# Kernel tuning notes

Hardware: AMD Instinct MI355X
Metric: run time of the kernel (lower is better)

Reference implementation:

```python
import jax, jax.numpy as jnp
import numpy as np

N, E = 50000, 1600000
IN_DIM, EMBED, OUT = 512, 128, 64


def setup_inputs() -> dict:
    key = jax.random.key(0)
    k = jax.random.split(key, 8)
    x = jax.random.normal(k[0], (N, IN_DIM), dtype=jnp.float32)
    edge_index = jax.random.randint(k[1], (2, E), 0, N, dtype=jnp.int32)
    W_dense = jax.random.normal(k[2], (EMBED, IN_DIM), dtype=jnp.float32) * 0.02
    b_dense = jnp.zeros((EMBED,), dtype=jnp.float32)
    W_gat = jax.random.normal(k[3], (OUT, EMBED), dtype=jnp.float32) * 0.05
    att_src = jax.random.normal(k[4], (OUT,), dtype=jnp.float32) * 0.1
    att_dst = jax.random.normal(k[5], (OUT,), dtype=jnp.float32) * 0.1
    b_gat = jnp.zeros((OUT,), dtype=jnp.float32)
    return {"x": x, "edge_index": edge_index, "W_dense": W_dense, "b_dense": b_dense,
            "W_gat": W_gat, "att_src": att_src, "att_dst": att_dst, "b_gat": b_gat}


def reference(x, edge_index, W_dense, b_dense, W_gat, att_src, att_dst, b_gat):
    # dense -> LeakyReLU(0.01) (nn.LeakyReLU default)
    h = jax.nn.leaky_relu(x @ W_dense.T + b_dense, negative_slope=0.01)  # [N, EMBED]
    n = h.shape[0]
    # GATConv (PyG, heads=1, add_self_loops=True, negative_slope=0.2)
    loops = jnp.arange(n, dtype=edge_index.dtype)
    src = jnp.concatenate([edge_index[0], loops])
    dst = jnp.concatenate([edge_index[1], loops])
    g = h @ W_gat.T  # [N, OUT]
    a_src = g @ att_src  # [N]
    a_dst = g @ att_dst  # [N]
    e = jax.nn.leaky_relu(a_src[src] + a_dst[dst], negative_slope=0.2)  # [E+N]
    # segment softmax over destination neighborhoods (self loops guarantee non-empty)
    m = jax.ops.segment_max(e, dst, num_segments=n)
    e = jnp.exp(e - m[dst])
    denom = jax.ops.segment_sum(e, dst, num_segments=n)
    alpha = e / denom[dst]
    out = jax.ops.segment_sum(g[src] * alpha[:, None], dst, num_segments=n) + b_gat
    # original returns ([embed_x], [embed_x]); we return the single embedding tensor
    return out
```

## Files before the change

### kernel.cpp

```cpp
#include <hip/hip_runtime.h>
#include <math.h>

#define IN_DIM 512
#define EMBED 128
#define OUT_DIM 64
#define NBPAD 256
#define SEGSH 12
#define CAP_LDS 10240

typedef __attribute__((ext_vector_type(8))) short bf16x8;
typedef __attribute__((ext_vector_type(4))) float f32x4;

__device__ __forceinline__ float lrelu(float v, float s) { return v > 0.f ? v : v * s; }

__device__ __forceinline__ float readlane_f(float v, int l) {
  return __int_as_float(__builtin_amdgcn_readlane(__float_as_int(v), l));
}

__device__ __forceinline__ unsigned short f2bf(float f) {
  unsigned int u = __float_as_uint(f);
  u += 0x7fff + ((u >> 16) & 1);
  return (unsigned short)(u >> 16);
}
__device__ __forceinline__ float bf2f(unsigned short h) {
  return __uint_as_float(((unsigned int)h) << 16);
}

__device__ __forceinline__ unsigned int cvt_pk_bf16(float a, float b) {
  unsigned int r;
  asm("v_cvt_pk_bf16_f32 %0, %1, %2" : "=v"(r) : "v"(a), "v"(b));
  return r;
}

#define LDA 40

__global__ __launch_bounds__(256) void split_w_kernel(
    const float* __restrict__ W, unsigned short* __restrict__ Wh,
    unsigned short* __restrict__ Wl, int total) {
  int i = (blockIdx.x * 256 + threadIdx.x) * 4;
  if (i >= total) return;
  float4 v = *(const float4*)(W + i);
  unsigned int h0 = cvt_pk_bf16(v.x, v.y);
  unsigned int h1 = cvt_pk_bf16(v.z, v.w);
  float r0 = v.x - __uint_as_float(h0 << 16);
  float r1 = v.y - __uint_as_float(h0 & 0xffff0000u);
  float r2 = v.z - __uint_as_float(h1 << 16);
  float r3 = v.w - __uint_as_float(h1 & 0xffff0000u);
  unsigned int l0 = cvt_pk_bf16(r0, r1);
  unsigned int l1 = cvt_pk_bf16(r2, r3);
  uint2 hh = make_uint2(h0, h1);
  uint2 ll = make_uint2(l0, l1);
  *(uint2*)(Wh + i) = hh;
  *(uint2*)(Wl + i) = ll;
}

__global__ __launch_bounds__(256) void gemm1_mfma_kernel(
    const float* __restrict__ x, const unsigned short* __restrict__ Wdh,
    const unsigned short* __restrict__ Wdl, const float* __restrict__ bd,
    float* __restrict__ h, int N) {
  __shared__ __align__(16) unsigned short Ah[64][LDA];
  __shared__ __align__(16) unsigned short Al[64][LDA];
  __shared__ __align__(16) unsigned short Bh[64][LDA];
  __shared__ __align__(16) unsigned short Bl[64][LDA];

  const int tid = threadIdx.x;
  const int lane = tid & 63;
  const int wid = tid >> 6;
  const int wr = wid >> 1, wc = wid & 1;
  const int mblk = blockIdx.x * 64;
  const int nblk = blockIdx.y * 64;
  const int quad = lane >> 4;
  const int l15 = lane & 15;

  const int arow = tid >> 2, acb = (tid & 3) * 8;
  const bool avalid = (mblk + arow) < N;
  const float* aptr = x + (size_t)(mblk + arow) * IN_DIM + acb;
  const unsigned short* bhp = Wdh + (size_t)(nblk + arow) * IN_DIM + acb;
  const unsigned short* blp = Wdl + (size_t)(nblk + arow) * IN_DIM + acb;

  f32x4 acc[2][2];
#pragma unroll
  for (int i = 0; i < 2; ++i)
#pragma unroll
    for (int j = 0; j < 2; ++j) acc[i][j] = (f32x4){0.f, 0.f, 0.f, 0.f};

  float4 t0, t1;
  uint4 bhv, blv;
  auto do_load = [&](int k0) {
    if (avalid) {
      t0 = *(const float4*)(aptr + k0);
      t1 = *(const float4*)(aptr + k0 + 4);
    } else {
      t0 = t1 = make_float4(0.f, 0.f, 0.f, 0.f);
    }
    bhv = *(const uint4*)(bhp + k0);
    blv = *(const uint4*)(blp + k0);
  };
  do_load(0);

  for (int k0 = 0; k0 < IN_DIM; k0 += 32) {
    float av[8] = {t0.x, t0.y, t0.z, t0.w, t1.x, t1.y, t1.z, t1.w};
    union { unsigned int u[4]; uint4 v; } AHI, ALO;
#pragma unroll
    for (int i = 0; i < 4; ++i) {
      unsigned int hp = cvt_pk_bf16(av[2 * i], av[2 * i + 1]);
      float r0 = av[2 * i] - __uint_as_float(hp << 16);
      float r1 = av[2 * i + 1] - __uint_as_float(hp & 0xffff0000u);
      AHI.u[i] = hp;
      ALO.u[i] = cvt_pk_bf16(r0, r1);
    }

    __syncthreads();
    *(uint4*)&Ah[arow][acb] = AHI.v;
    *(uint4*)&Al[arow][acb] = ALO.v;
    *(uint4*)&Bh[arow][acb] = bhv;
    *(uint4*)&Bl[arow][acb] = blv;
    __syncthreads();

    if (k0 + 32 < IN_DIM) do_load(k0 + 32);

    bf16x8 ah[2], al[2], bh[2], bl[2];
#pragma unroll
    for (int mi = 0; mi < 2; ++mi) {
      int r = wr * 32 + mi * 16 + l15;
      ah[mi] = *(const bf16x8*)&Ah[r][quad * 8];
      al[mi] = *(const bf16x8*)&Al[r][quad * 8];
    }
#pragma unroll
    for (int ni = 0; ni < 2; ++ni) {
      int r = wc * 32 + ni * 16 + l15;
      bh[ni] = *(const bf16x8*)&Bh[r][quad * 8];
      bl[ni] = *(const bf16x8*)&Bl[r][quad * 8];
    }
#pragma unroll
    for (int mi = 0; mi < 2; ++mi)
#pragma unroll
      for (int ni = 0; ni < 2; ++ni) {
        acc[mi][ni] = __builtin_amdgcn_mfma_f32_16x16x32_bf16(ah[mi], bh[ni], acc[mi][ni], 0, 0, 0);
        acc[mi][ni] = __builtin_amdgcn_mfma_f32_16x16x32_bf16(al[mi], bh[ni], acc[mi][ni], 0, 0, 0);
        acc[mi][ni] = __builtin_amdgcn_mfma_f32_16x16x32_bf16(ah[mi], bl[ni], acc[mi][ni], 0, 0, 0);
      }
  }

#pragma unroll
  for (int mi = 0; mi < 2; ++mi)
#pragma unroll
    for (int ni = 0; ni < 2; ++ni) {
      int n = nblk + wc * 32 + ni * 16 + l15;
      float b = bd[n];
#pragma unroll
      for (int r = 0; r < 4; ++r) {
        int m = mblk + wr * 32 + mi * 16 + quad * 4 + r;
        if (m < N) h[(size_t)m * EMBED + n] = lrelu(acc[mi][ni][r] + b, 0.01f);
      }
    }
}

__global__ __launch_bounds__(256) void gemm2_mfma_kernel(
    const float* __restrict__ h, const float* __restrict__ Wg,
    const float* __restrict__ att_src, const float* __restrict__ att_dst,
    float* __restrict__ g, float* __restrict__ a_src, float* __restrict__ a_dst,
    int N) {
  __shared__ __align__(16) unsigned short Ah[128][LDA];
  __shared__ __align__(16) unsigned short Al[128][LDA];
  __shared__ __align__(16) unsigned short Bh[64][LDA];
  __shared__ __align__(16) unsigned short Bl[64][LDA];

  const int tid = threadIdx.x;
  const int lane = tid & 63;
  const int wid = tid >> 6;
  const int wr = wid >> 1, wc = wid & 1;
  const int mblk = blockIdx.x * 128;
  const int quad = lane >> 4;
  const int l15 = lane & 15;

  const int arow = tid >> 1, acb = (tid & 1) * 16;
  const int brow = tid >> 2, bcb = (tid & 3) * 8;
  const bool avalid = (mblk + arow) < N;
  const float* aptr = h + (size_t)(mblk + arow) * EMBED + acb;
  const float* bptr = Wg + (size_t)brow * EMBED + bcb;

  f32x4 acc[4][2];
#pragma unroll
  for (int i = 0; i < 4; ++i)
#pragma unroll
    for (int j = 0; j < 2; ++j) acc[i][j] = (f32x4){0.f, 0.f, 0.f, 0.f};

  float4 t0, t1, t2, t3, u0, u1;
  auto do_load = [&](int k0) {
    if (avalid) {
      t0 = *(const float4*)(aptr + k0);
      t1 = *(const float4*)(aptr + k0 + 4);
      t2 = *(const float4*)(aptr + k0 + 8);
      t3 = *(const float4*)(aptr + k0 + 12);
    } else {
      t0 = t1 = t2 = t3 = make_float4(0.f, 0.f, 0.f, 0.f);
    }
    u0 = *(const float4*)(bptr + k0);
    u1 = *(const float4*)(bptr + k0 + 4);
  };
  do_load(0);

  for (int k0 = 0; k0 < EMBED; k0 += 32) {
    float av[16] = {t0.x, t0.y, t0.z, t0.w, t1.x, t1.y, t1.z, t1.w,
                    t2.x, t2.y, t2.z, t2.w, t3.x, t3.y, t3.z, t3.w};
    union { unsigned short us[16]; uint4 v[2]; } AH, AL;
#pragma unroll
    for (int i = 0; i < 16; ++i) {
      unsigned short hi = f2bf(av[i]);
      AH.us[i] = hi;
      AL.us[i] = f2bf(av[i] - bf2f(hi));
    }
    float bv[8] = {u0.x, u0.y, u0.z, u0.w, u1.x, u1.y, u1.z, u1.w};
    union { unsigned short us[8]; uint4 v; } BH, BL;
#pragma unroll
    for (int i = 0; i < 8; ++i) {
      unsigned short hi = f2bf(bv[i]);
      BH.us[i] = hi;
      BL.us[i] = f2bf(bv[i] - bf2f(hi));
    }

    __syncthreads();
    *(uint4*)&Ah[arow][acb] = AH.v[0];
    *(uint4*)&Ah[arow][acb + 8] = AH.v[1];
    *(uint4*)&Al[arow][acb] = AL.v[0];
    *(uint4*)&Al[arow][acb + 8] = AL.v[1];
    *(uint4*)&Bh[brow][bcb] = BH.v;
    *(uint4*)&Bl[brow][bcb] = BL.v;
    __syncthreads();

    if (k0 + 32 < EMBED) do_load(k0 + 32);

    bf16x8 ah[4], al[4], bh[2], bl[2];
#pragma unroll
    for (int mi = 0; mi < 4; ++mi) {
      int r = wr * 64 + mi * 16 + l15;
      ah[mi] = *(const bf16x8*)&Ah[r][quad * 8];
      al[mi] = *(const bf16x8*)&Al[r][quad * 8];
    }
#pragma unroll
    for (int ni = 0; ni < 2; ++ni) {
      int r = wc * 32 + ni * 16 + l15;
      bh[ni] = *(const bf16x8*)&Bh[r][quad * 8];
      bl[ni] = *(const bf16x8*)&Bl[r][quad * 8];
    }
#pragma unroll
    for (int mi = 0; mi < 4; ++mi)
#pragma unroll
      for (int ni = 0; ni < 2; ++ni) {
        acc[mi][ni] = __builtin_amdgcn_mfma_f32_16x16x32_bf16(ah[mi], bh[ni], acc[mi][ni], 0, 0, 0);
        acc[mi][ni] = __builtin_amdgcn_mfma_f32_16x16x32_bf16(al[mi], bh[ni], acc[mi][ni], 0, 0, 0);
        acc[mi][ni] = __builtin_amdgcn_mfma_f32_16x16x32_bf16(ah[mi], bl[ni], acc[mi][ni], 0, 0, 0);
      }
  }

  float as_[2], ad_[2];
#pragma unroll
  for (int ni = 0; ni < 2; ++ni) {
    int n = wc * 32 + ni * 16 + l15;
    as_[ni] = att_src[n];
    ad_[ni] = att_dst[n];
  }
#pragma unroll
  for (int mi = 0; mi < 4; ++mi) {
#pragma unroll
    for (int r = 0; r < 4; ++r) {
      int m = mblk + wr * 64 + mi * 16 + quad * 4 + r;
      float ps = acc[mi][0][r] * as_[0] + acc[mi][1][r] * as_[1];
      float pd = acc[mi][0][r] * ad_[0] + acc[mi][1][r] * ad_[1];
#pragma unroll
      for (int d = 1; d < 16; d <<= 1) {
        ps += __shfl_xor(ps, d, 64);
        pd += __shfl_xor(pd, d, 64);
      }
      if (m < N) {
#pragma unroll
        for (int ni = 0; ni < 2; ++ni) {
          int n = wc * 32 + ni * 16 + l15;
          g[(size_t)m * OUT_DIM + n] = acc[mi][ni][r];
        }
        if (l15 == 0 && wc == 0) {
          a_src[m] = ps;
          a_dst[m] = pd;
        }
      }
    }
  }
  __syncthreads();
#pragma unroll
  for (int mi = 0; mi < 4; ++mi) {
#pragma unroll
    for (int r = 0; r < 4; ++r) {
      int m = mblk + wr * 64 + mi * 16 + quad * 4 + r;
      float ps = acc[mi][0][r] * as_[0] + acc[mi][1][r] * as_[1];
      float pd = acc[mi][0][r] * ad_[0] + acc[mi][1][r] * ad_[1];
#pragma unroll
      for (int d = 1; d < 16; d <<= 1) {
        ps += __shfl_xor(ps, d, 64);
        pd += __shfl_xor(pd, d, 64);
      }
      if (m < N && l15 == 0 && wc == 1) {
        atomicAdd(&a_src[m], ps);
        atomicAdd(&a_dst[m], pd);
      }
    }
  }
}

__global__ __launch_bounds__(256) void hist_count_kernel(
    const int* __restrict__ ei, int* __restrict__ histT, int nblkP, int E,
    int N) {
  __shared__ int cnt[NBPAD];
  const int t = threadIdx.x;
  cnt[t] = 0;
  __syncthreads();
  const int T = E + N;
  const int base = blockIdx.x << SEGSH;
#pragma unroll
  for (int q = 0; q < (1 << SEGSH) / 256; ++q) {
    int i = base + q * 256 + t;
    if (i < T) {
      int d = (i < E) ? ei[E + i] : (i - E);
      atomicAdd(&cnt[d >> 8], 1);
    }
  }
  __syncthreads();
  histT[(size_t)t * nblkP + blockIdx.x] = cnt[t];
}

__global__ __launch_bounds__(256) void row_scan_kernel(
    int* __restrict__ histT, int* __restrict__ bucket_tot, int nblkP) {
  __shared__ int sc[256];
  const int t = threadIdx.x;
  int* row = histT + (size_t)blockIdx.x * nblkP;
  const int per = (nblkP + 255) / 256;
  int loc[8];
  int sum = 0;
#pragma unroll 4
  for (int j = 0; j < per; ++j) {
    int idx = t * per + j;
    int v = (idx < nblkP) ? row[idx] : 0;
    loc[j] = sum;
    sum += v;
  }
  sc[t] = sum;
  __syncthreads();
  for (int dlt = 1; dlt < 256; dlt <<= 1) {
    int add = (t >= dlt) ? sc[t - dlt] : 0;
    __syncthreads();
    sc[t] += add;
    __syncthreads();
  }
  const int off = sc[t] - sum;
#pragma unroll 4
  for (int j = 0; j < per; ++j) {
    int idx = t * per + j;
    if (idx < nblkP) row[idx] = off + loc[j];
  }
  if (t == 255) bucket_tot[blockIdx.x] = sc[255];
}

__global__ __launch_bounds__(256) void base_scan_kernel(
    const int* __restrict__ bucket_tot, int* __restrict__ bucket_base,
    int* __restrict__ offsets, int N, int T) {
  __shared__ int sc[256];
  const int t = threadIdx.x;
  int v = bucket_tot[t];
  sc[t] = v;
  __syncthreads();
  for (int dlt = 1; dlt < 256; dlt <<= 1) {
    int add = (t >= dlt) ? sc[t - dlt] : 0;
    __syncthreads();
    sc[t] += add;
    __syncthreads();
  }
  bucket_base[t] = sc[t] - v;
  if (t == 0) offsets[N] = T;
}

__global__ __launch_bounds__(256) void bin_kernel(
    const int* __restrict__ ei, const int* __restrict__ histT,
    const int* __restrict__ bucket_base, int* __restrict__ stageB, int nblkP,
    int E, int N) {
  __shared__ int cnt[NBPAD];
  __shared__ int basev[NBPAD];
  const int t = threadIdx.x;
  cnt[t] = 0;
  basev[t] = bucket_base[t] + histT[(size_t)t * nblkP + blockIdx.x];
  __syncthreads();
  const int T = E + N;
  const int base = blockIdx.x << SEGSH;
#pragma unroll
  for (int q = 0; q < (1 << SEGSH) / 256; ++q) {
    int i = base + q * 256 + t;
    if (i < T) {
      int s, d;
      if (i < E) {
        s = ei[i];
        d = ei[E + i];
      } else {
        s = d = i - E;
      }
      int b = d >> 8;
      int r = atomicAdd(&cnt[b], 1);
      stageB[basev[b] + r] = (s << 8) | (d & 255);
    }
  }
}

__global__ __launch_bounds__(256) void build_kernel(
    const int* __restrict__ stageB, const int* __restrict__ bucket_base,
    const int* __restrict__ bucket_tot, const float* __restrict__ a_src,
    const float* __restrict__ a_dst, int* __restrict__ offsets,
    int2* __restrict__ csr_pack, int N) {
  __shared__ int cnt[256];
  __shared__ int pre[256];
  __shared__ int cur[256];
  __shared__ int2 buf[CAP_LDS];
  const int b = blockIdx.x;
  const int t = threadIdx.x;
  const int base = bucket_base[b];
  const int tot = bucket_tot[b];
  cnt[t] = 0;
  __syncthreads();
  const int* sp = stageB + base;
  for (int i = t; i < tot; i += 256) atomicAdd(&cnt[sp[i] & 255], 1);
  __syncthreads();
  int v = cnt[t];
  pre[t] = v;
  __syncthreads();
  for (int dlt = 1; dlt < 256; dlt <<= 1) {
    int add = (t >= dlt) ? pre[t - dlt] : 0;
    __syncthreads();
    pre[t] += add;
    __syncthreads();
  }
  const int excl = pre[t] - v;
  cur[t] = excl;
  const int d_self = (b << 8) | t;
  if (d_self < N) offsets[d_self] = base + excl;
  __syncthreads();
  for (int i = t; i < tot; i += 256) {
    int rec = sp[i];
    int dl = rec & 255;
    int s = rec >> 8;
    float e = a_src[s] + a_dst[(b << 8) | dl];
    e = e > 0.f ? e : 0.2f * e;
    int pos = atomicAdd(&cur[dl], 1);
    int2 r2 = make_int2(s, __float_as_int(e));
    if (pos < CAP_LDS)
      buf[pos] = r2;
    else
      csr_pack[base + pos] = r2;
  }
  __syncthreads();
  const int lim = min(tot, CAP_LDS);
  for (int i = t; i < lim; i += 256) csr_pack[base + i] = buf[i];
}

__global__ __launch_bounds__(256) void aggregate_kernel(
    const int* __restrict__ offsets, const int2* __restrict__ csr_pack,
    const float* __restrict__ g, const float* __restrict__ b_gat,
    float* __restrict__ out, int N) {
  const int lane = threadIdx.x & 63;
  const int node = blockIdx.x * 4 + (threadIdx.x >> 6);
  if (node >= N) return;
  const int beg = offsets[node], end = offsets[node + 1];

  float m = -1e30f;
  for (int j = beg + lane; j < end; j += 64)
    m = fmaxf(m, __int_as_float(csr_pack[j].y));
#pragma unroll
  for (int d = 1; d < 64; d <<= 1) m = fmaxf(m, __shfl_xor(m, d, 64));

  float l = 0.f;
  for (int j = beg + lane; j < end; j += 64)
    l += __expf(__int_as_float(csr_pack[j].y) - m);
#pragma unroll
  for (int d = 1; d < 64; d <<= 1) l += __shfl_xor(l, d, 64);
  const float inv_l = 1.f / l;

  float acc0 = 0.f, acc1 = 0.f, acc2 = 0.f, acc3 = 0.f;
  for (int jb = beg; jb < end; jb += 64) {
    int j = jb + lane;
    float p = 0.f;
    int s = 0;
    if (j < end) {
      int2 rec = csr_pack[j];
      p = __expf(__int_as_float(rec.y) - m) * inv_l;
      s = rec.x;
    }
    const int cnt = min(64, end - jb);
    int jj = 0;
    for (; jj + 4 <= cnt; jj += 4) {
      int s0 = __builtin_amdgcn_readlane(s, jj);
      int s1 = __builtin_amdgcn_readlane(s, jj + 1);
      int s2 = __builtin_amdgcn_readlane(s, jj + 2);
      int s3 = __builtin_amdgcn_readlane(s, jj + 3);
      float p0 = readlane_f(p, jj);
      float p1 = readlane_f(p, jj + 1);
      float p2 = readlane_f(p, jj + 2);
      float p3 = readlane_f(p, jj + 3);
      acc0 += p0 * g[((size_t)s0 << 6) + lane];
      acc1 += p1 * g[((size_t)s1 << 6) + lane];
      acc2 += p2 * g[((size_t)s2 << 6) + lane];
      acc3 += p3 * g[((size_t)s3 << 6) + lane];
    }
    for (; jj < cnt; ++jj) {
      int s0 = __builtin_amdgcn_readlane(s, jj);
      float p0 = readlane_f(p, jj);
      acc0 += p0 * g[((size_t)s0 << 6) + lane];
    }
  }
  out[(size_t)node * OUT_DIM + lane] = (acc0 + acc1) + (acc2 + acc3) + b_gat[lane];
}

extern "C" void kernel_launch(void* const* d_in, const int* in_sizes, int n_in,
                              void* d_out, int out_size, void* d_ws, size_t ws_size,
                              hipStream_t stream) {
  const float* x = (const float*)d_in[0];
  const int* ei = (const int*)d_in[1];
  const float* Wd = (const float*)d_in[2];
  const float* bd = (const float*)d_in[3];
  const float* Wg = (const float*)d_in[4];
  const float* att_src = (const float*)d_in[5];
  const float* att_dst = (const float*)d_in[6];
  const float* bg = (const float*)d_in[7];
  float* out = (float*)d_out;

  const int N = in_sizes[0] / IN_DIM;
  const int E = in_sizes[1] / 2;
  const int T = E + N;
  const int NB = (N + 255) >> 8;
  const int nblkP = (T + (1 << SEGSH) - 1) >> SEGSH;

  char* ws = (char*)d_ws;
  size_t off = 0;
  auto alloc = [&](size_t bytes) -> void* {
    void* p = ws + off;
    off += (bytes + 15) & ~(size_t)15;
    return p;
  };
  float* h = (float*)alloc((size_t)N * EMBED * 4);
  float* g = (float*)alloc((size_t)N * OUT_DIM * 4);
  float* a_src = (float*)alloc((size_t)N * 4);
  float* a_dst = (float*)alloc((size_t)N * 4);
  int* offsets = (int*)alloc((size_t)(N + 1) * 4);
  int* histT = (int*)alloc((size_t)NBPAD * nblkP * 4);
  int* bucket_base = (int*)alloc((size_t)NBPAD * 4);
  int* bucket_tot = (int*)alloc((size_t)NBPAD * 4);
  int* stageB = (int*)alloc((size_t)T * 4);
  int2* csr_pack = (int2*)alloc((size_t)T * 8);
  unsigned short* Wdh = (unsigned short*)alloc((size_t)EMBED * IN_DIM * 2);
  unsigned short* Wdl = (unsigned short*)alloc((size_t)EMBED * IN_DIM * 2);

  const int WTOT = EMBED * IN_DIM;
  hipLaunchKernelGGL(split_w_kernel, dim3(WTOT / 1024), dim3(256), 0, stream,
                     Wd, Wdh, Wdl, WTOT);
  hipLaunchKernelGGL(gemm1_mfma_kernel, dim3((N + 63) / 64, 2), dim3(256), 0,
                     stream, x, Wdh, Wdl, bd, h, N);
  hipLaunchKernelGGL(gemm2_mfma_kernel, dim3((N + 127) / 128), dim3(256), 0,
                     stream, h, Wg, att_src, att_dst, g, a_src, a_dst, N);
  hipLaunchKernelGGL(hist_count_kernel, dim3(nblkP), dim3(256), 0, stream,
                     ei, histT, nblkP, E, N);
  hipLaunchKernelGGL(row_scan_kernel, dim3(NBPAD), dim3(256), 0, stream,
                     histT, bucket_tot, nblkP);
  hipLaunchKernelGGL(base_scan_kernel, dim3(1), dim3(256), 0, stream,
                     bucket_tot, bucket_base, offsets, N, T);
  hipLaunchKernelGGL(bin_kernel, dim3(nblkP), dim3(256), 0, stream,
                     ei, histT, bucket_base, stageB, nblkP, E, N);
  hipLaunchKernelGGL(build_kernel, dim3(NB), dim3(256), 0, stream,
                     stageB, bucket_base, bucket_tot, a_src, a_dst, offsets,
                     csr_pack, N);
  hipLaunchKernelGGL(aggregate_kernel, dim3((N + 3) / 4), dim3(256), 0, stream,
                     offsets, csr_pack, g, bg, out, N);
}
```

Before: 329.9 us.

## Preload full weight slice into swizzled LDS and stream A from registers in gemm1

The first GEMM now copies each block's whole 64-column slice of the split bf16 weights (hi and lo) into 128KB of XOR-swizzled shared memory once. Each wave then loads its x rows straight from global memory into registers in MFMA operand layout, so the per-step LDS staging and the two barriers per K step are gone. The block grows to 512 threads covering 128 rows, and the K loop is fully unrolled with the next A tile prefetched in registers. The cost is very high LDS use per block, which limits occupancy to about one block per CU, plus less coalesced per-lane global reads of x.

Result: slower. 366.8 us (+11.2%).

```diff
diff --git a/kernel.cpp b/kernel.cpp
--- a/kernel.cpp
+++ b/kernel.cpp
@@ -54,29 +54,55 @@
   *(uint2*)(Wl + i) = ll;
 }
 
-__global__ __launch_bounds__(256) void gemm1_mfma_kernel(
+__global__ __launch_bounds__(512) void gemm1_mfma_kernel(
     const float* __restrict__ x, const unsigned short* __restrict__ Wdh,
     const unsigned short* __restrict__ Wdl, const float* __restrict__ bd,
     float* __restrict__ h, int N) {
-  __shared__ __align__(16) unsigned short Ah[64][LDA];
-  __shared__ __align__(16) unsigned short Al[64][LDA];
-  __shared__ __align__(16) unsigned short Bh[64][LDA];
-  __shared__ __align__(16) unsigned short Bl[64][LDA];
+  __shared__ __align__(16) unsigned char Bsm[131072];
 
   const int tid = threadIdx.x;
   const int lane = tid & 63;
   const int wid = tid >> 6;
-  const int wr = wid >> 1, wc = wid & 1;
-  const int mblk = blockIdx.x * 64;
+  const int wr = wid >> 1;
+  const int wc = wid & 1;
+  const int mblk = blockIdx.x * 128;
   const int nblk = blockIdx.y * 64;
   const int quad = lane >> 4;
   const int l15 = lane & 15;
 
-  const int arow = tid >> 2, acb = (tid & 3) * 8;
-  const bool avalid = (mblk + arow) < N;
-  const float* aptr = x + (size_t)(mblk + arow) * IN_DIM + acb;
-  const unsigned short* bhp = Wdh + (size_t)(nblk + arow) * IN_DIM + acb;
-  const unsigned short* blp = Wdl + (size_t)(nblk + arow) * IN_DIM + acb;
+  int r0g = mblk + wr * 32 + l15;
+  int r1g = r0g + 16;
+  int r0c = r0g < N ? r0g : N - 1;
+  int r1c = r1g < N ? r1g : N - 1;
+  const float* ap0 = x + (size_t)r0c * IN_DIM + quad * 8;
+  const float* ap1 = x + (size_t)r1c * IN_DIM + quad * 8;
+
+  float4 t0a, t0b, t1a, t1b;
+  auto load_step = [&](int k0) {
+    t0a = *(const float4*)(ap0 + k0);
+    t0b = *(const float4*)(ap0 + k0 + 4);
+    t1a = *(const float4*)(ap1 + k0);
+    t1b = *(const float4*)(ap1 + k0 + 4);
+  };
+  load_step(0);
+
+  {
+    const int o = tid * 128;
+    const int row = o >> 10;
+    const int colb = o & 1023;
+    const unsigned short* srch = Wdh + (size_t)(nblk + row) * IN_DIM;
+    const unsigned short* srcl = Wdl + (size_t)(nblk + row) * IN_DIM;
+    const int sw = (row & 7) << 4;
+#pragma unroll
+    for (int c = 0; c < 8; ++c) {
+      int byte = colb + c * 16;
+      uint4 vh = *(const uint4*)((const char*)srch + byte);
+      uint4 vl = *(const uint4*)((const char*)srcl + byte);
+      int dst = (row << 10) | (byte ^ sw);
+      *(uint4*)(Bsm + dst) = vh;
+      *(uint4*)(Bsm + 65536 + dst) = vl;
+    }
+  }
 
   f32x4 acc[2][2];
 #pragma unroll
@@ -84,62 +110,55 @@
 #pragma unroll
     for (int j = 0; j < 2; ++j) acc[i][j] = (f32x4){0.f, 0.f, 0.f, 0.f};
 
-  float4 t0, t1;
-  uint4 bhv, blv;
-  auto do_load = [&](int k0) {
-    if (avalid) {
-      t0 = *(const float4*)(aptr + k0);
-      t1 = *(const float4*)(aptr + k0 + 4);
-    } else {
-      t0 = t1 = make_float4(0.f, 0.f, 0.f, 0.f);
-    }
-    bhv = *(const uint4*)(bhp + k0);
-    blv = *(const uint4*)(blp + k0);
-  };
-  do_load(0);
-
-  for (int k0 = 0; k0 < IN_DIM; k0 += 32) {
-    float av[8] = {t0.x, t0.y, t0.z, t0.w, t1.x, t1.y, t1.z, t1.w};
-    union { unsigned int u[4]; uint4 v; } AHI, ALO;
+  const int brow0 = wc * 32 + l15;
+  const int sw = (brow0 & 7) << 4;
+  const int qx = (quad << 4) ^ (sw & 48);
+  const int s6 = sw & 64;
+  const unsigned char* pH = Bsm + (brow0 << 10);
+  const unsigned char* pL = pH + 65536;
+
+  __syncthreads();
+
+#pragma unroll
+  for (int s = 0; s < IN_DIM / 32; ++s) {
+    const int k0 = s * 32;
+    float a0[8] = {t0a.x, t0a.y, t0a.z, t0a.w, t0b.x, t0b.y, t0b.z, t0b.w};
+    float a1[8] = {t1a.x, t1a.y, t1a.z, t1a.w, t1b.x, t1b.y, t1b.z, t1b.w};
+    union { unsigned int u[4]; bf16x8 v; } H0, L0, H1, L1;
 #pragma unroll
     for (int i = 0; i < 4; ++i) {
-      unsigned int hp = cvt_pk_bf16(av[2 * i], av[2 * i + 1]);
-      float r0 = av[2 * i] - __uint_as_float(hp << 16);
-      float r1 = av[2 * i + 1] - __uint_as_float(hp & 0xffff0000u);
-      AHI.u[i] = hp;
-      ALO.u[i] = cvt_pk_bf16(r0, r1);
-    }
-
-    __syncthreads();
-    *(uint4*)&Ah[arow][acb] = AHI.v;
-    *(uint4*)&Al[arow][acb] = ALO.v;
-    *(uint4*)&Bh[arow][acb] = bhv;
-    *(uint4*)&Bl[arow][acb] = blv;
-    __syncthreads();
-
-    if (k0 + 32 < IN_DIM) do_load(k0 + 32);
-
-    bf16x8 ah[2], al[2], bh[2], bl[2];
-#pragma unroll
-    for (int mi = 0; mi < 2; ++mi) {
-      int r = wr * 32 + mi * 16 + l15;
-      ah[mi] = *(const bf16x8*)&Ah[r][quad * 8];
-      al[mi] = *(const bf16x8*)&Al[r][quad * 8];
-    }
-#pragma unroll
-    for (int ni = 0; ni < 2; ++ni) {
-      int r = wc * 32 + ni * 16 + l15;
-      bh[ni] = *(const bf16x8*)&Bh[r][quad * 8];
-      bl[ni] = *(const bf16x8*)&Bl[r][quad * 8];
-    }
-#pragma unroll
-    for (int mi = 0; mi < 2; ++mi)
-#pragma unroll
-      for (int ni = 0; ni < 2; ++ni) {
-        acc[mi][ni] = __builtin_amdgcn_mfma_f32_16x16x32_bf16(ah[mi], bh[ni], acc[mi][ni], 0, 0, 0);
-        acc[mi][ni] = __builtin_amdgcn_mfma_f32_16x16x32_bf16(al[mi], bh[ni], acc[mi][ni], 0, 0, 0);
-        acc[mi][ni] = __builtin_amdgcn_mfma_f32_16x16x32_bf16(ah[mi], bl[ni], acc[mi][ni], 0, 0, 0);
-      }
+      unsigned int hp0 = cvt_pk_bf16(a0[2 * i], a0[2 * i + 1]);
+      float q0 = a0[2 * i] - __uint_as_float(hp0 << 16);
+      float q1 = a0[2 * i + 1] - __uint_as_float(hp0 & 0xffff0000u);
+      H0.u[i] = hp0;
+      L0.u[i] = cvt_pk_bf16(q0, q1);
+      unsigned int hp1 = cvt_pk_bf16(a1[2 * i], a1[2 * i + 1]);
+      float q2 = a1[2 * i] - __uint_as_float(hp1 << 16);
+      float q3 = a1[2 * i + 1] - __uint_as_float(hp1 & 0xffff0000u);
+      H1.u[i] = hp1;
+      L1.u[i] = cvt_pk_bf16(q2, q3);
+    }
+
+    if (s + 1 < IN_DIM / 32) load_step(k0 + 32);
+
+    const int vb = ((k0 << 1) ^ s6) | qx;
+    bf16x8 bh0 = *(const bf16x8*)(pH + vb);
+    bf16x8 bh1 = *(const bf16x8*)(pH + vb + (16 << 10));
+    bf16x8 bl0 = *(const bf16x8*)(pL + vb);
+    bf16x8 bl1 = *(const bf16x8*)(pL + vb + (16 << 10));
+
+    acc[0][0] = __builtin_amdgcn_mfma_f32_16x16x32_bf16(H0.v, bh0, acc[0][0], 0, 0, 0);
+    acc[0][0] = __builtin_amdgcn_mfma_f32_16x16x32_bf16(L0.v, bh0, acc[0][0], 0, 0, 0);
+    acc[0][0] = __builtin_amdgcn_mfma_f32_16x16x32_bf16(H0.v, bl0, acc[0][0], 0, 0, 0);
+    acc[0][1] = __builtin_amdgcn_mfma_f32_16x16x32_bf16(H0.v, bh1, acc[0][1], 0, 0, 0);
+    acc[0][1] = __builtin_amdgcn_mfma_f32_16x16x32_bf16(L0.v, bh1, acc[0][1], 0, 0, 0);
+    acc[0][1] = __builtin_amdgcn_mfma_f32_16x16x32_bf16(H0.v, bl1, acc[0][1], 0, 0, 0);
+    acc[1][0] = __builtin_amdgcn_mfma_f32_16x16x32_bf16(H1.v, bh0, acc[1][0], 0, 0, 0);
+    acc[1][0] = __builtin_amdgcn_mfma_f32_16x16x32_bf16(L1.v, bh0, acc[1][0], 0, 0, 0);
+    acc[1][0] = __builtin_amdgcn_mfma_f32_16x16x32_bf16(H1.v, bl0, acc[1][0], 0, 0, 0);
+    acc[1][1] = __builtin_amdgcn_mfma_f32_16x16x32_bf16(H1.v, bh1, acc[1][1], 0, 0, 0);
+    acc[1][1] = __builtin_amdgcn_mfma_f32_16x16x32_bf16(L1.v, bh1, acc[1][1], 0, 0, 0);
+    acc[1][1] = __builtin_amdgcn_mfma_f32_16x16x32_bf16(H1.v, bl1, acc[1][1], 0, 0, 0);
   }
 
 #pragma unroll
@@ -557,7 +576,7 @@
   const int WTOT = EMBED * IN_DIM;
   hipLaunchKernelGGL(split_w_kernel, dim3(WTOT / 1024), dim3(256), 0, stream,
                      Wd, Wdh, Wdl, WTOT);
-  hipLaunchKernelGGL(gemm1_mfma_kernel, dim3((N + 63) / 64, 2), dim3(256), 0,
+  hipLaunchKernelGGL(gemm1_mfma_kernel, dim3((N + 127) / 128, 2), dim3(512), 0,
                      stream, x, Wdh, Wdl, bd, h, N);
   hipLaunchKernelGGL(gemm2_mfma_kernel, dim3((N + 127) / 128), dim3(256), 0,
                      stream, h, Wg, att_src, att_dst, g, a_src, a_dst, N);
```

## Retile gemm1 to 128x128 blocks with direct global-to-LDS loads and swizzle

Applied to the files above, without the earlier changes.

The first GEMM now computes a full 128-row by 128-column output tile per block, so x is read from global memory once instead of twice across the two N-blocks. Tiles are loaded with global_load_lds straight into XOR-swizzled shared memory, skipping the register staging. The fp32 x tile is kept in LDS and split into bf16 hi/lo per wave at fragment-read time. In exchange the kernel holds more accumulator registers (16 MFMA tiles per wave), uses more LDS, and no longer prefetches the next k-slice, so load latency is no longer hidden behind compute.

Result: faster. 315.9 us (-4.2%).

```diff
diff --git a/kernel.cpp b/kernel.cpp
--- a/kernel.cpp
+++ b/kernel.cpp
@@ -30,6 +30,12 @@
   unsigned int r;
   asm("v_cvt_pk_bf16_f32 %0, %1, %2" : "=v"(r) : "v"(a), "v"(b));
   return r;
+}
+
+__device__ __forceinline__ void gl_lds16(const void* g, void* l) {
+  __builtin_amdgcn_global_load_lds(
+      (const __attribute__((address_space(1))) unsigned int*)g,
+      (__attribute__((address_space(3))) unsigned int*)l, 16, 0, 0);
 }
 
 #define LDA 40
@@ -58,99 +64,127 @@
     const float* __restrict__ x, const unsigned short* __restrict__ Wdh,
     const unsigned short* __restrict__ Wdl, const float* __restrict__ bd,
     float* __restrict__ h, int N) {
-  __shared__ __align__(16) unsigned short Ah[64][LDA];
-  __shared__ __align__(16) unsigned short Al[64][LDA];
-  __shared__ __align__(16) unsigned short Bh[64][LDA];
-  __shared__ __align__(16) unsigned short Bl[64][LDA];
+  __shared__ __align__(16) unsigned char Afp[16384];
+  __shared__ __align__(16) unsigned char Bhs[8192];
+  __shared__ __align__(16) unsigned char Bls[8192];
 
   const int tid = threadIdx.x;
   const int lane = tid & 63;
   const int wid = tid >> 6;
-  const int wr = wid >> 1, wc = wid & 1;
-  const int mblk = blockIdx.x * 64;
-  const int nblk = blockIdx.y * 64;
+  const int mblk = blockIdx.x * 128;
   const int quad = lane >> 4;
   const int l15 = lane & 15;
 
-  const int arow = tid >> 2, acb = (tid & 3) * 8;
-  const bool avalid = (mblk + arow) < N;
-  const float* aptr = x + (size_t)(mblk + arow) * IN_DIM + acb;
-  const unsigned short* bhp = Wdh + (size_t)(nblk + arow) * IN_DIM + acb;
-  const unsigned short* blp = Wdl + (size_t)(nblk + arow) * IN_DIM + acb;
-
-  f32x4 acc[2][2];
+  const char* asrc[4];
+  void* adst[4];
+#pragma unroll
+  for (int i = 0; i < 4; ++i) {
+    int chunk = i * 256 + tid;
+    int row = chunk >> 3, ch = chunk & 7;
+    int rg = mblk + row;
+    if (rg >= N) rg = N - 1;
+    asrc[i] = (const char*)x + (size_t)rg * (IN_DIM * 4) + ((ch ^ (row & 7)) << 4);
+    adst[i] = Afp + chunk * 16;
+  }
+  const char* bsrcH[2];
+  const char* bsrcL[2];
+  void* bdstH[2];
+  void* bdstL[2];
+#pragma unroll
+  for (int i = 0; i < 2; ++i) {
+    int chunk = i * 256 + tid;
+    int row = chunk >> 2, ch = chunk & 3;
+    int cs = ch ^ ((row >> 1) & 3);
+    size_t srcoff = (size_t)row * (IN_DIM * 2) + (cs << 4);
+    bsrcH[i] = (const char*)Wdh + srcoff;
+    bsrcL[i] = (const char*)Wdl + srcoff;
+    bdstH[i] = Bhs + chunk * 16;
+    bdstL[i] = Bls + chunk * 16;
+  }
+
+  f32x4 acc[2][8];
 #pragma unroll
   for (int i = 0; i < 2; ++i)
 #pragma unroll
-    for (int j = 0; j < 2; ++j) acc[i][j] = (f32x4){0.f, 0.f, 0.f, 0.f};
-
-  float4 t0, t1;
-  uint4 bhv, blv;
-  auto do_load = [&](int k0) {
-    if (avalid) {
-      t0 = *(const float4*)(aptr + k0);
-      t1 = *(const float4*)(aptr + k0 + 4);
-    } else {
-      t0 = t1 = make_float4(0.f, 0.f, 0.f, 0.f);
-    }
-    bhv = *(const uint4*)(bhp + k0);
-    blv = *(const uint4*)(blp + k0);
-  };
-  do_load(0);
+    for (int j = 0; j < 8; ++j) acc[i][j] = (f32x4){0.f, 0.f, 0.f, 0.f};
+
+  int aoff[2][2];
+#pragma unroll
+  for (int mi = 0; mi < 2; ++mi) {
+    int row = wid * 32 + mi * 16 + l15;
+    int sw = (row & 7) << 4;
+#pragma unroll
+    for (int hf = 0; hf < 2; ++hf)
+      aoff[mi][hf] = row * 128 + (((quad << 5) | (hf << 4)) ^ sw);
+  }
+  int boff[8];
+#pragma unroll
+  for (int ni = 0; ni < 8; ++ni) {
+    int row = ni * 16 + l15;
+    boff[ni] = row * 64 + ((quad ^ ((row >> 1) & 3)) << 4);
+  }
 
   for (int k0 = 0; k0 < IN_DIM; k0 += 32) {
-    float av[8] = {t0.x, t0.y, t0.z, t0.w, t1.x, t1.y, t1.z, t1.w};
-    union { unsigned int u[4]; uint4 v; } AHI, ALO;
-#pragma unroll
-    for (int i = 0; i < 4; ++i) {
-      unsigned int hp = cvt_pk_bf16(av[2 * i], av[2 * i + 1]);
-      float r0 = av[2 * i] - __uint_as_float(hp << 16);
-      float r1 = av[2 * i + 1] - __uint_as_float(hp & 0xffff0000u);
-      AHI.u[i] = hp;
-      ALO.u[i] = cvt_pk_bf16(r0, r1);
-    }
-
-    __syncthreads();
-    *(uint4*)&Ah[arow][acb] = AHI.v;
-    *(uint4*)&Al[arow][acb] = ALO.v;
-    *(uint4*)&Bh[arow][acb] = bhv;
-    *(uint4*)&Bl[arow][acb] = blv;
-    __syncthreads();
-
-    if (k0 + 32 < IN_DIM) do_load(k0 + 32);
-
-    bf16x8 ah[2], al[2], bh[2], bl[2];
+    __syncthreads();
+    const size_t ka = (size_t)k0 * 4;
+    const size_t kb = (size_t)k0 * 2;
+#pragma unroll
+    for (int i = 0; i < 4; ++i) gl_lds16(asrc[i] + ka, adst[i]);
+#pragma unroll
+    for (int i = 0; i < 2; ++i) {
+      gl_lds16(bsrcH[i] + kb, bdstH[i]);
+      gl_lds16(bsrcL[i] + kb, bdstL[i]);
+    }
+    __syncthreads();
+
+    bf16x8 AH[2], AL[2];
 #pragma unroll
     for (int mi = 0; mi < 2; ++mi) {
-      int r = wr * 32 + mi * 16 + l15;
-      ah[mi] = *(const bf16x8*)&Ah[r][quad * 8];
-      al[mi] = *(const bf16x8*)&Al[r][quad * 8];
-    }
-#pragma unroll
-    for (int ni = 0; ni < 2; ++ni) {
-      int r = wc * 32 + ni * 16 + l15;
-      bh[ni] = *(const bf16x8*)&Bh[r][quad * 8];
-      bl[ni] = *(const bf16x8*)&Bl[r][quad * 8];
-    }
-#pragma unroll
-    for (int mi = 0; mi < 2; ++mi)
-#pragma unroll
-      for (int ni = 0; ni < 2; ++ni) {
-        acc[mi][ni] = __builtin_amdgcn_mfma_f32_16x16x32_bf16(ah[mi], bh[ni], acc[mi][ni], 0, 0, 0);
-        acc[mi][ni] = __builtin_amdgcn_mfma_f32_16x16x32_bf16(al[mi], bh[ni], acc[mi][ni], 0, 0, 0);
-        acc[mi][ni] = __builtin_amdgcn_mfma_f32_16x16x32_bf16(ah[mi], bl[ni], acc[mi][ni], 0, 0, 0);
-      }
+      float4 f0 = *(const float4*)(Afp + aoff[mi][0]);
+      float4 f1 = *(const float4*)(Afp + aoff[mi][1]);
+      float av[8] = {f0.x, f0.y, f0.z, f0.w, f1.x, f1.y, f1.z, f1.w};
+      union { unsigned int u[4]; bf16x8 v; } H, L;
+#pragma unroll
+      for (int i = 0; i < 4; ++i) {
+        unsigned int hp = cvt_pk_bf16(av[2 * i], av[2 * i + 1]);
+        float q0 = av[2 * i] - __uint_as_float(hp << 16);
+        float q1 = av[2 * i + 1] - __uint_as_float(hp & 0xffff0000u);
+        H.u[i] = hp;
+        L.u[i] = cvt_pk_bf16(q0, q1);
+      }
+      AH[mi] = H.v;
+      AL[mi] = L.v;
+    }
+
+#pragma unroll
+    for (int hf = 0; hf < 2; ++hf) {
+      bf16x8 BH[4], BL[4];
+#pragma unroll
+      for (int j = 0; j < 4; ++j) {
+        BH[j] = *(const bf16x8*)(Bhs + boff[hf * 4 + j]);
+        BL[j] = *(const bf16x8*)(Bls + boff[hf * 4 + j]);
+      }
+#pragma unroll
+      for (int mi = 0; mi < 2; ++mi)
+#pragma unroll
+        for (int j = 0; j < 4; ++j) {
+          int ni = hf * 4 + j;
+          acc[mi][ni] = __builtin_amdgcn_mfma_f32_16x16x32_bf16(AH[mi], BH[j], acc[mi][ni], 0, 0, 0);
+          acc[mi][ni] = __builtin_amdgcn_mfma_f32_16x16x32_bf16(AL[mi], BH[j], acc[mi][ni], 0, 0, 0);
+          acc[mi][ni] = __builtin_amdgcn_mfma_f32_16x16x32_bf16(AH[mi], BL[j], acc[mi][ni], 0, 0, 0);
+        }
+    }
   }
 
 #pragma unroll
   for (int mi = 0; mi < 2; ++mi)
 #pragma unroll
-    for (int ni = 0; ni < 2; ++ni) {
-      int n = nblk + wc * 32 + ni * 16 + l15;
+    for (int ni = 0; ni < 8; ++ni) {
+      int n = ni * 16 + l15;
       float b = bd[n];
 #pragma unroll
       for (int r = 0; r < 4; ++r) {
-        int m = mblk + wr * 32 + mi * 16 + quad * 4 + r;
+        int m = mblk + wid * 32 + mi * 16 + quad * 4 + r;
         if (m < N) h[(size_t)m * EMBED + n] = lrelu(acc[mi][ni][r] + b, 0.01f);
       }
     }
@@ -557,7 +591,7 @@
   const int WTOT = EMBED * IN_DIM;
   hipLaunchKernelGGL(split_w_kernel, dim3(WTOT / 1024), dim3(256), 0, stream,
                      Wd, Wdh, Wdl, WTOT);
-  hipLaunchKernelGGL(gemm1_mfma_kernel, dim3((N + 63) / 64, 2), dim3(256), 0,
+  hipLaunchKernelGGL(gemm1_mfma_kernel, dim3((N + 127) / 128), dim3(256), 0,
                      stream, x, Wdh, Wdl, bd, h, N);
   hipLaunchKernelGGL(gemm2_mfma_kernel, dim3((N + 127) / 128), dim3(256), 0,
                      stream, h, Wg, att_src, att_dst, g, a_src, a_dst, N);
```
